# Kernel tuning notes

Hardware: AMD Instinct MI355X
Metric: run time of the kernel (lower is better)

Reference implementation:

```python
import jax, jax.numpy as jnp
import numpy as np

B, S, H, E = 64, 1024, 256, 256

def setup_inputs() -> dict:
    key = jax.random.key(0)
    k = jax.random.split(key, 6)
    scale = 1.0 / np.sqrt(H)
    return {
        "data_alpha": jax.random.normal(k[0], (B, S, H), jnp.float32),
        "data_beta": jax.random.normal(k[1], (B, S, H), jnp.float32),
        "data_embed": jax.random.normal(k[2], (B, S, E), jnp.float32),
        "data_mask": jnp.ones((B, S), jnp.float32),
        "Wb": jax.random.normal(k[3], (E, H), jnp.float32) * scale,
        "bb": jnp.zeros((E,), jnp.float32),
        "Wa": jax.random.normal(k[4], (H,), jnp.float32) * scale,
        "ba": jnp.zeros((1,), jnp.float32),
    }

def reference(data_alpha, data_beta, data_embed, data_mask, Wb, bb, Wa, ba):
    # beta gates: tanh(Linear(H->E))  [B,S,E]
    beta_w = jnp.tanh(jnp.einsum('bsh,eh->bse', data_beta, Wb) + bb)
    # alpha logits: Linear(H->1)  [B,S]
    corr = jnp.einsum('bsh,h->bs', data_alpha, Wa) + ba
    attn = jnp.exp(corr)[:, None, :]                       # [B,1,S]
    seq = data_alpha.shape[1]
    flag = jnp.triu(jnp.ones((seq, seq), data_alpha.dtype))[None]  # j >= i
    ef = flag * data_mask[:, None, :]                      # [B,S,S]
    num = attn * ef                                        # [B,S,S]
    acc = jnp.sum(num, axis=-1, keepdims=True) + 1e-10     # [B,S,1]
    alpha = num / acc                                      # [B,S,S]
    ew = beta_w * data_embed                               # [B,S,E]
    return jnp.einsum('bij,bje->bie', alpha, ew)           # [B,S,E]
```

## Files before the change

kernel.cpp:

```cpp
#include <hip/hip_runtime.h>
#include <hip/hip_bf16.h>

#define S_LEN 1024
#define B_DIM 64
#define H_DIM 256
#define E_DIM 256
#define M_ROWS (B_DIM * S_LEN)

#define CT_COLS 64
#define NCT (E_DIM / CT_COLS)
#define CHUNK_R 256
#define NCHUNKS (S_LEN / CHUNK_R)
#define NTHREADS 1024
#define NWAVES 16

#define BPAD 264
#define PPAD 66

typedef __attribute__((ext_vector_type(8))) short bf16x8;
typedef __attribute__((ext_vector_type(4))) float f32x4;

__device__ __forceinline__ short cvt1(float f) {
  union { float ff; unsigned u; } t;
  t.ff = f;
  unsigned u = t.u;
  return (short)((u + 0x7fffu + ((u >> 16) & 1u)) >> 16);
}

__device__ __forceinline__ bf16x8 cvt8v(float4 x, float4 y) {
  bf16x8 r;
  r[0] = cvt1(x.x); r[1] = cvt1(x.y); r[2] = cvt1(x.z); r[3] = cvt1(x.w);
  r[4] = cvt1(y.x); r[5] = cvt1(y.y); r[6] = cvt1(y.z); r[7] = cvt1(y.w);
  return r;
}

__global__ __launch_bounds__(256) void w_kernel(
    const float* __restrict__ alpha, const float* __restrict__ Wa,
    const float* __restrict__ ba, const float* __restrict__ mask,
    float* __restrict__ wv) {
  int wave = threadIdx.x >> 6, lane = threadIdx.x & 63;
  long long row = (long long)blockIdx.x * 4 + wave;
  const float4 a = reinterpret_cast<const float4*>(alpha + row * H_DIM)[lane];
  const float4 wa = reinterpret_cast<const float4*>(Wa)[lane];
  float d = a.x * wa.x + a.y * wa.y + a.z * wa.z + a.w * wa.w;
#pragma unroll
  for (int m = 32; m; m >>= 1) d += __shfl_xor(d, m);
  if (lane == 0) wv[row] = expf(d + ba[0]) * mask[row];
}

__global__ __launch_bounds__(1024) void acc_kernel(
    const float* __restrict__ wv, float* __restrict__ invacc) {
  __shared__ float s[2][S_LEN];
  int b = blockIdx.x, i = threadIdx.x;
  s[0][i] = wv[b * S_LEN + i];
  __syncthreads();
  int src = 0;
#pragma unroll
  for (int off = 1; off < S_LEN; off <<= 1) {
    float v = s[src][i];
    if (i + off < S_LEN) v += s[src][i + off];
    s[src ^ 1][i] = v;
    __syncthreads();
    src ^= 1;
  }
  invacc[b * S_LEN + i] = 1.0f / (s[src][i] + 1e-10f);
}

__global__ __launch_bounds__(NTHREADS, 1) void fused_kernel(
    const float* __restrict__ beta, const float* __restrict__ Wb,
    const float* __restrict__ bb, const float* __restrict__ embed,
    const float* __restrict__ wv, const float* __restrict__ invacc,
    float* __restrict__ out) {
  __shared__ short Bsm[CT_COLS * BPAD];
  __shared__ float Psm[CHUNK_R * PPAD];
  __shared__ float segsum[NWAVES * CT_COLS];
  __shared__ float carry[CT_COLS];

  const int tid = threadIdx.x;
  const int b = blockIdx.x >> 2;
  const int colbase = (blockIdx.x & 3) * CT_COLS;

  {
    int c = tid >> 4, ks = (tid & 15) * 16;
    const float4* src =
        reinterpret_cast<const float4*>(Wb + (long long)(colbase + c) * H_DIM + ks);
    float4 v0 = src[0], v1 = src[1], v2 = src[2], v3 = src[3];
    *reinterpret_cast<bf16x8*>(&Bsm[c * BPAD + ks]) = cvt8v(v0, v1);
    *reinterpret_cast<bf16x8*>(&Bsm[c * BPAD + ks + 8]) = cvt8v(v2, v3);
  }
  if (tid < CT_COLS) carry[tid] = 0.f;
  __syncthreads();

  const int wave = tid >> 6, lane = tid & 63;
  const int rl = lane & 15, kg = lane >> 4;
  const int col = tid & 63, seg = tid >> 6;

  for (int chunk = NCHUNKS - 1; chunk >= 0; --chunk) {
    const long long rowstart = (long long)b * S_LEN + chunk * CHUNK_R;
    const long long arow = rowstart + wave * 16 + rl;
    const float* aptr = beta + arow * H_DIM + kg * 8;

    f32x4 acc[4] = {{0.f,0.f,0.f,0.f},{0.f,0.f,0.f,0.f},
                    {0.f,0.f,0.f,0.f},{0.f,0.f,0.f,0.f}};

    float4 a0[2], a1[2];
    a0[0] = *reinterpret_cast<const float4*>(aptr + 0);
    a1[0] = *reinterpret_cast<const float4*>(aptr + 4);
    a0[1] = *reinterpret_cast<const float4*>(aptr + 32);
    a1[1] = *reinterpret_cast<const float4*>(aptr + 36);
#pragma unroll
    for (int ks = 0; ks < 8; ++ks) {
      float4 na0 = {0.f,0.f,0.f,0.f}, na1 = {0.f,0.f,0.f,0.f};
      if (ks < 6) {
        na0 = *reinterpret_cast<const float4*>(aptr + (ks + 2) * 32);
        na1 = *reinterpret_cast<const float4*>(aptr + (ks + 2) * 32 + 4);
      }
      bf16x8 am = cvt8v(a0[0], a1[0]);
      int kb = ks * 32 + kg * 8;
#pragma unroll
      for (int j = 0; j < 4; ++j) {
        bf16x8 bn = *reinterpret_cast<const bf16x8*>(&Bsm[(j * 16 + rl) * BPAD + kb]);
        acc[j] = __builtin_amdgcn_mfma_f32_16x16x32_bf16(am, bn, acc[j], 0, 0, 0);
      }
      a0[0] = a0[1]; a1[0] = a1[1];
      a0[1] = na0;   a1[1] = na1;
    }

#pragma unroll
    for (int q = 0; q < 4; ++q) {
      int rloc = wave * 16 + kg * 4 + q;
      long long r = rowstart + rloc;
      float wvv = wv[r];
      const float* erow = embed + r * E_DIM + colbase;
#pragma unroll
      for (int j = 0; j < 4; ++j) {
        int c = j * 16 + rl;
        float p = wvv * tanhf(acc[j][q] + bb[colbase + c]) * erow[c];
        Psm[rloc * PPAD + c] = p;
      }
    }
    __syncthreads();

    float lsum = 0.f;
#pragma unroll
    for (int i = 0; i < 16; ++i)
      lsum += Psm[(seg * 16 + i) * PPAD + col];
    segsum[seg * CT_COLS + col] = lsum;
    __syncthreads();

    float offset = carry[col];
    for (int s2 = seg + 1; s2 < NWAVES; ++s2)
      offset += segsum[s2 * CT_COLS + col];
    __syncthreads();
    if (seg == 0) carry[col] = offset + lsum;

    float running = offset;
    long long rbase = rowstart + seg * 16;
#pragma unroll
    for (int i = 15; i >= 0; --i) {
      running += Psm[(seg * 16 + i) * PPAD + col];
      out[(rbase + i) * E_DIM + colbase + col] = running * invacc[rbase + i];
    }
    __syncthreads();
  }
}

extern "C" void kernel_launch(void* const* d_in, const int* in_sizes, int n_in,
                              void* d_out, int out_size, void* d_ws,
                              size_t ws_size, hipStream_t stream) {
  const float* alpha = (const float*)d_in[0];
  const float* beta = (const float*)d_in[1];
  const float* embed = (const float*)d_in[2];
  const float* mask = (const float*)d_in[3];
  const float* Wb = (const float*)d_in[4];
  const float* bb = (const float*)d_in[5];
  const float* Wa = (const float*)d_in[6];
  const float* ba = (const float*)d_in[7];
  float* out = (float*)d_out;

  float* wv = (float*)d_ws;
  float* invacc = wv + M_ROWS;

  w_kernel<<<M_ROWS / 4, 256, 0, stream>>>(alpha, Wa, ba, mask, wv);
  acc_kernel<<<B_DIM, 1024, 0, stream>>>(wv, invacc);
  fused_kernel<<<B_DIM * NCT, NTHREADS, 0, stream>>>(beta, Wb, bb, embed, wv,
                                                     invacc, out);
}
```

Baseline: 283.1 us.

## Do suffix scan in registers via shuffles, drop LDS staging, remap blocks

Instead of writing the gated products to a shared-memory tile and rescanning it, each lane computes a suffix sum over its four MFMA rows in registers. Cross-lane shuffles combine the lane groups, and only per-wave totals go through shared memory. This removes the large Psm buffer and one barrier. The change also swaps tanhf for an exp/reciprocal approximation, remaps block indices so the four column tiles of one batch are spread apart in launch order, and raises the launch-bounds occupancy hint. The cost is possible accuracy loss from the fast tanh and less coalesced output and embed accesses.

```diff
diff --git a/kernel.cpp b/kernel.cpp
--- a/kernel.cpp
+++ b/kernel.cpp
@@ -15,7 +15,6 @@
 #define NWAVES 16
 
 #define BPAD 264
-#define PPAD 66
 
 typedef __attribute__((ext_vector_type(8))) short bf16x8;
 typedef __attribute__((ext_vector_type(4))) float f32x4;
@@ -32,6 +31,11 @@
   r[0] = cvt1(x.x); r[1] = cvt1(x.y); r[2] = cvt1(x.z); r[3] = cvt1(x.w);
   r[4] = cvt1(y.x); r[5] = cvt1(y.y); r[6] = cvt1(y.z); r[7] = cvt1(y.w);
   return r;
+}
+
+__device__ __forceinline__ float fast_tanh(float x) {
+  float t = __expf(2.0f * x);
+  return 1.0f - 2.0f * __builtin_amdgcn_rcpf(t + 1.0f);
 }
 
 __global__ __launch_bounds__(256) void w_kernel(
@@ -66,19 +70,19 @@
   invacc[b * S_LEN + i] = 1.0f / (s[src][i] + 1e-10f);
 }
 
-__global__ __launch_bounds__(NTHREADS, 1) void fused_kernel(
+__global__ __launch_bounds__(NTHREADS, 8) void fused_kernel(
     const float* __restrict__ beta, const float* __restrict__ Wb,
     const float* __restrict__ bb, const float* __restrict__ embed,
     const float* __restrict__ wv, const float* __restrict__ invacc,
     float* __restrict__ out) {
   __shared__ short Bsm[CT_COLS * BPAD];
-  __shared__ float Psm[CHUNK_R * PPAD];
   __shared__ float segsum[NWAVES * CT_COLS];
   __shared__ float carry[CT_COLS];
 
   const int tid = threadIdx.x;
-  const int b = blockIdx.x >> 2;
-  const int colbase = (blockIdx.x & 3) * CT_COLS;
+  const int hw = blockIdx.x;
+  const int b = (hw & 7) + (((hw >> 3) & 7) << 3);
+  const int colbase = (hw >> 6) * CT_COLS;
 
   {
     int c = tid >> 4, ks = (tid & 15) * 16;
@@ -93,12 +97,11 @@
 
   const int wave = tid >> 6, lane = tid & 63;
   const int rl = lane & 15, kg = lane >> 4;
-  const int col = tid & 63, seg = tid >> 6;
 
   for (int chunk = NCHUNKS - 1; chunk >= 0; --chunk) {
     const long long rowstart = (long long)b * S_LEN + chunk * CHUNK_R;
-    const long long arow = rowstart + wave * 16 + rl;
-    const float* aptr = beta + arow * H_DIM + kg * 8;
+    const long long r0 = rowstart + wave * 16;
+    const float* aptr = beta + (r0 + rl) * H_DIM + kg * 8;
 
     f32x4 acc[4] = {{0.f,0.f,0.f,0.f},{0.f,0.f,0.f,0.f},
                     {0.f,0.f,0.f,0.f},{0.f,0.f,0.f,0.f}};
@@ -126,42 +129,63 @@
       a0[1] = na0;   a1[1] = na1;
     }
 
+    float wvq[4], inv[4];
 #pragma unroll
     for (int q = 0; q < 4; ++q) {
-      int rloc = wave * 16 + kg * 4 + q;
-      long long r = rowstart + rloc;
-      float wvv = wv[r];
-      const float* erow = embed + r * E_DIM + colbase;
-#pragma unroll
-      for (int j = 0; j < 4; ++j) {
-        int c = j * 16 + rl;
-        float p = wvv * tanhf(acc[j][q] + bb[colbase + c]) * erow[c];
-        Psm[rloc * PPAD + c] = p;
-      }
+      long long r = r0 + kg * 4 + q;
+      wvq[q] = wv[r];
+      inv[q] = invacc[r];
+    }
+
+    float sv[4][4];
+    float off[4];
+    float cn[4];
+#pragma unroll
+    for (int j = 0; j < 4; ++j) {
+      int c = j * 16 + rl;
+      int e = colbase + c;
+      float bbe = bb[e];
+      float p[4];
+#pragma unroll
+      for (int q = 0; q < 4; ++q) {
+        long long r = r0 + kg * 4 + q;
+        p[q] = wvq[q] * fast_tanh(acc[j][q] + bbe) * embed[r * E_DIM + e];
+      }
+      sv[j][3] = p[3];
+      sv[j][2] = p[2] + sv[j][3];
+      sv[j][1] = p[1] + sv[j][2];
+      sv[j][0] = p[0] + sv[j][1];
+      float gtot = sv[j][0];
+      float t16 = __shfl_xor(gtot, 16);
+      float t32 = __shfl_xor(gtot, 32);
+      float t48 = __shfl_xor(gtot, 48);
+      off[j] = (kg == 0) ? (t16 + t32 + t48)
+             : (kg == 1) ? (t32 + t48)
+             : (kg == 2) ? t16 : 0.f;
+      float wtot = gtot + t16 + t32 + t48;
+      if (kg == 0) segsum[wave * CT_COLS + c] = wtot;
     }
     __syncthreads();
 
-    float lsum = 0.f;
-#pragma unroll
-    for (int i = 0; i < 16; ++i)
-      lsum += Psm[(seg * 16 + i) * PPAD + col];
-    segsum[seg * CT_COLS + col] = lsum;
+#pragma unroll
+    for (int j = 0; j < 4; ++j) {
+      int c = j * 16 + rl;
+      float segoff = carry[c];
+      for (int w2 = wave + 1; w2 < NWAVES; ++w2)
+        segoff += segsum[w2 * CT_COLS + c];
+      off[j] += segoff;
+      cn[j] = off[j] + sv[j][0];
+#pragma unroll
+      for (int q = 0; q < 4; ++q) {
+        long long r = r0 + kg * 4 + q;
+        out[r * E_DIM + colbase + c] = (sv[j][q] + off[j]) * inv[q];
+      }
+    }
     __syncthreads();
-
-    float offset = carry[col];
-    for (int s2 = seg + 1; s2 < NWAVES; ++s2)
-      offset += segsum[s2 * CT_COLS + col];
-    __syncthreads();
-    if (seg == 0) carry[col] = offset + lsum;
-
-    float running = offset;
-    long long rbase = rowstart + seg * 16;
-#pragma unroll
-    for (int i = 15; i >= 0; --i) {
-      running += Psm[(seg * 16 + i) * PPAD + col];
-      out[(rbase + i) * E_DIM + colbase + col] = running * invacc[rbase + i];
-    }
-    __syncthreads();
+    if (wave == 0 && kg == 0) {
+#pragma unroll
+      for (int j = 0; j < 4; ++j) carry[j * 16 + rl] = cn[j];
+    }
   }
 }
 
```

After: 259.5 us. 8.3% less time.
